# Kernel optimization log

Hardware: AMD Instinct MI355X
Metric: run time of the kernel (lower is better)

## Reference

```python
import jax, jax.numpy as jnp
import numpy as np

N, D_IN, D_OUT = 4096, 1024, 1024
DROPOUT_RATE = 0.1


def setup_inputs() -> dict:
    key = jax.random.key(0)
    kx, kq, kk, kv = jax.random.split(key, 4)
    s = 1.0 / np.sqrt(D_IN)
    return {
        "x": jax.random.normal(kx, (N, D_IN), dtype=jnp.float32),
        "wq": jax.random.normal(kq, (D_OUT, D_IN), dtype=jnp.float32) * s,
        "wk": jax.random.normal(kk, (D_OUT, D_IN), dtype=jnp.float32) * s,
        "wv": jax.random.normal(kv, (D_OUT, D_IN), dtype=jnp.float32) * s,
    }


def reference(x, wq, wk, wv):
    # torch Linear: y = x @ W.T  (no bias since qkv_bias=False)
    q = x @ wq.T                      # [N, d_out]
    k = x @ wk.T
    v = x @ wv.T
    scores = q @ k.T                  # [N, N]
    n = scores.shape[0]
    causal = jnp.tril(jnp.ones((n, n), dtype=bool))  # keep lower triangle
    masked = jnp.where(causal, scores, -jnp.inf)
    scale = k.shape[-1] ** 0.5
    weights = jax.nn.softmax(masked / scale, axis=-1)
    # dropout (train mode), fixed key for determinism
    keep = jax.random.bernoulli(jax.random.key(42), 1.0 - DROPOUT_RATE, weights.shape)
    weights = jnp.where(keep, weights / (1.0 - DROPOUT_RATE), 0.0)
    return weights @ v                # [N, d_out]
```

## Files before the change

### kernel.cpp

```cpp
#include <hip/hip_runtime.h>
#include <hip/hip_fp16.h>

typedef __attribute__((ext_vector_type(8))) _Float16 f16x8;
typedef __attribute__((ext_vector_type(4))) float f32x4;

typedef const __attribute__((address_space(1))) void gas_void;
typedef __attribute__((address_space(3))) void las_void;
typedef __attribute__((address_space(3))) const __half las_chalf;

__device__ __forceinline__ f16x8 ldsr(const __half* p) {
    f16x8 r;
    asm volatile("ds_read_b128 %0, %1" : "=v"(r) : "v"((las_chalf*)p));
    return r;
}

__global__ __launch_bounds__(256) void cast_f32_f16_k(const float* __restrict__ in,
                                                      __half* __restrict__ out, int n) {
    int i = (blockIdx.x * 256 + threadIdx.x) * 8;
    if (i >= n) return;
    float4 a = *(const float4*)(in + i);
    float4 b = *(const float4*)(in + i + 4);
    __half2 h[4] = { __floats2half2_rn(a.x, a.y), __floats2half2_rn(a.z, a.w),
                     __floats2half2_rn(b.x, b.y), __floats2half2_rn(b.z, b.w) };
    *(int4*)(out + i) = *(int4*)h;
}

__global__ __launch_bounds__(256) void cast3_f32_f16_k(const float* __restrict__ a,
                                                       const float* __restrict__ b,
                                                       const float* __restrict__ c,
                                                       __half* __restrict__ out) {
    const int which = blockIdx.x >> 9;
    const float* src = which == 0 ? a : (which == 1 ? b : c);
    const int i = (((blockIdx.x & 511) * 256) + threadIdx.x) * 8;
    float4 va = *(const float4*)(src + i);
    float4 vb = *(const float4*)(src + i + 4);
    __half2 h[4] = { __floats2half2_rn(va.x, va.y), __floats2half2_rn(va.z, va.w),
                     __floats2half2_rn(vb.x, vb.y), __floats2half2_rn(vb.z, vb.w) };
    *(int4*)(out + (size_t)which * 1048576 + i) = *(int4*)h;
}

__global__ __launch_bounds__(256) void transpose_f16_k(const __half* __restrict__ in,
                                                       __half* __restrict__ out,
                                                       int R, int ldin) {
    __shared__ __half t[64][72];
    int r0 = blockIdx.x * 64, c0 = blockIdx.y * 64;
    for (int idx = threadIdx.x; idx < 64 * 64; idx += 256) {
        int r = idx >> 6, c = idx & 63;
        t[r][c] = in[(size_t)(r0 + r) * ldin + c0 + c];
    }
    __syncthreads();
    for (int idx = threadIdx.x; idx < 64 * 64; idx += 256) {
        int r = idx >> 6, c = idx & 63;
        out[(size_t)(c0 + r) * R + r0 + c] = t[c][r];
    }
}

__device__ __forceinline__ void storeC(__half* C, size_t off, float v) { C[off] = __float2half(v); }
__device__ __forceinline__ void storeC(float*  C, size_t off, float v) { C[off] = v; }

template <typename CT, bool LOWER_ONLY, bool SPLITK>
__global__ __launch_bounds__(512, 2)
void gemm256(const __half* __restrict__ A, const __half* __restrict__ B, CT* __restrict__ C,
             float* __restrict__ P1, float* __restrict__ P2, float* __restrict__ P3,
             int lda, int ldb, int ldc, int NTin, float scale) {
    int bi, c = 0;
    const int bj = blockIdx.y;
    if (SPLITK) {
        int x = blockIdx.x;
        if (x < 4)       { bi = x;                    c = 0; }
        else if (x < 12) { bi = 4  + ((x - 4) >> 1);  c = (x - 4) & 1; }
        else if (x < 24) { bi = 8  + (x - 12) / 3;    c = (x - 12) % 3; }
        else             { bi = 12 + ((x - 24) >> 2); c = (x - 24) & 3; }
    } else {
        bi = blockIdx.x;
        if (LOWER_ONLY && bj > bi) return;
    }
    const int brow = bi * 256, bcol = bj * 256;
    const int tid = threadIdx.x;
    const int lane = tid & 63, wid = tid >> 6;
    const int wm = wid >> 2, wn = wid & 3;
    const int lane15 = lane & 15;
    const int kxor = (lane & 7) << 3;
    const int g16 = (lane >> 4) << 3;

    int k_lo = 0, NT = NTin;
    if (SPLITK) { int full = 4 * (bi + 1); k_lo = c * 16; NT = min(full - k_lo, 16); }

    extern __shared__ __half smem[];

    const int srow = (wid << 3) + (lane >> 3);
    const int scol = ((lane & 7) ^ ((lane >> 3) & 7)) << 3;

    auto stage_half = [&](const __half* G, int ldg, int growbase, int kt, int buf, int mat, int half) {
        const __half* src = G + (size_t)(growbase + half * 128 + srow) * ldg + kt * 64 + scol;
        __half* dst = &smem[buf * 32768 + mat * 16384 + (half * 128 + (wid << 3)) * 64];
        __builtin_amdgcn_global_load_lds((gas_void*)src, (las_void*)dst, 16, 0, 0);
        __builtin_amdgcn_global_load_lds((gas_void*)(src + (size_t)64 * ldg),
                                         (las_void*)(dst + 64 * 64), 16, 0, 0);
    };

    f32x4 acc[8][4] = {};
    f16x8 bfrag[2][4];

    stage_half(B, ldb, bcol, k_lo, 0, 1, 0);
    stage_half(B, ldb, bcol, k_lo, 0, 1, 1);
    stage_half(A, lda, brow, k_lo, 0, 0, 0);
    stage_half(A, lda, brow, k_lo, 0, 0, 1);
    if (NT > 1) {
        stage_half(B, ldb, bcol, k_lo + 1, 1, 1, 0);
        stage_half(B, ldb, bcol, k_lo + 1, 1, 1, 1);
    }

    for (int Tr = 0; Tr < NT; ++Tr) {
        const int Ta = k_lo + Tr;
        const int buf = Tr & 1;
        const __half* Abase = &smem[buf * 32768 + (wm * 128 + lane15) * 64];
        const __half* Bbase = &smem[buf * 32768 + 16384 + (wn * 64 + lane15) * 64];

        if (Tr < NT - 1) asm volatile("s_waitcnt vmcnt(4)" ::: "memory");
        else             asm volatile("s_waitcnt vmcnt(0)" ::: "memory");
        __builtin_amdgcn_s_barrier();

        {
#pragma unroll
            for (int kk = 0; kk < 2; ++kk)
#pragma unroll
                for (int n = 0; n < 4; ++n)
                    bfrag[kk][n] = ldsr(Bbase + (n * 16) * 64 + ((kk * 32 + g16) ^ kxor));
            f16x8 af[2][2];
#pragma unroll
            for (int mi = 0; mi < 2; ++mi)
#pragma unroll
                for (int kk = 0; kk < 2; ++kk)
                    af[mi][kk] = ldsr(Abase + (mi * 16) * 64 + ((kk * 32 + g16) ^ kxor));
            if (Tr + 1 < NT) stage_half(A, lda, brow, Ta + 1, buf ^ 1, 0, 0);
            asm volatile("s_waitcnt lgkmcnt(0)" ::: "memory");
            __builtin_amdgcn_sched_barrier(0);
            __builtin_amdgcn_s_setprio(1);
#pragma unroll
            for (int mi = 0; mi < 2; ++mi)
#pragma unroll
                for (int n = 0; n < 4; ++n)
#pragma unroll
                    for (int kk = 0; kk < 2; ++kk)
                        acc[mi][n] = __builtin_amdgcn_mfma_f32_16x16x32_f16(
                            af[mi][kk], bfrag[kk][n], acc[mi][n], 0, 0, 0);
            __builtin_amdgcn_s_setprio(0);
            __builtin_amdgcn_s_barrier();
        }

#pragma unroll
        for (int p = 1; p < 4; ++p) {
            f16x8 af[2][2];
#pragma unroll
            for (int mi = 0; mi < 2; ++mi)
#pragma unroll
                for (int kk = 0; kk < 2; ++kk)
                    af[mi][kk] = ldsr(Abase + ((2 * p + mi) * 16) * 64 + ((kk * 32 + g16) ^ kxor));
            if (p == 1)      { if (Tr + 1 < NT) stage_half(A, lda, brow, Ta + 1, buf ^ 1, 0, 1); }
            else if (p == 2) { if (Tr + 2 < NT) stage_half(B, ldb, bcol, Ta + 2, buf, 1, 0); }
            else             { if (Tr + 2 < NT) stage_half(B, ldb, bcol, Ta + 2, buf, 1, 1); }
            asm volatile("s_waitcnt lgkmcnt(0)" ::: "memory");
            __builtin_amdgcn_sched_barrier(0);
            __builtin_amdgcn_s_setprio(1);
#pragma unroll
            for (int mi = 0; mi < 2; ++mi)
#pragma unroll
                for (int n = 0; n < 4; ++n)
#pragma unroll
                    for (int kk = 0; kk < 2; ++kk)
                        acc[2 * p + mi][n] = __builtin_amdgcn_mfma_f32_16x16x32_f16(
                            af[mi][kk], bfrag[kk][n], acc[2 * p + mi][n], 0, 0, 0);
            __builtin_amdgcn_s_setprio(0);
            __builtin_amdgcn_s_barrier();
        }
    }

    CT* Ct = C;
    if (SPLITK && c > 0) Ct = (CT*)(c == 1 ? P1 : (c == 2 ? P2 : P3));
    const int r0 = (lane >> 4) << 2;
#pragma unroll
    for (int m = 0; m < 8; ++m) {
#pragma unroll
        for (int n = 0; n < 4; ++n) {
            int col = bcol + wn * 64 + n * 16 + lane15;
#pragma unroll
            for (int r = 0; r < 4; ++r) {
                int row = brow + wm * 128 + m * 16 + r0 + r;
                storeC(Ct, (size_t)row * ldc + col, acc[m][n][r] * scale);
            }
        }
    }
}

__global__ __launch_bounds__(256) void pv_reduce_k(float* __restrict__ out,
                                                   const float* __restrict__ P1,
                                                   const float* __restrict__ P2,
                                                   const float* __restrict__ P3) {
    const int row = 1024 + blockIdx.x;
    const size_t o = (size_t)row * 1024 + threadIdx.x * 4;
    float4 s = *(float4*)(out + o);
    float4 a = *(const float4*)(P1 + o);
    s.x += a.x; s.y += a.y; s.z += a.z; s.w += a.w;
    if (row >= 2048) {
        float4 b = *(const float4*)(P2 + o);
        s.x += b.x; s.y += b.y; s.z += b.z; s.w += b.w;
    }
    if (row >= 3072) {
        float4 d = *(const float4*)(P3 + o);
        s.x += d.x; s.y += d.y; s.z += d.z; s.w += d.w;
    }
    *(float4*)(out + o) = s;
}

__device__ __forceinline__ uint32_t rotl32(uint32_t x, int d) { return (x << d) | (x >> (32 - d)); }

__device__ __forceinline__ bool keep_bit(uint32_t i, uint32_t j) {
    uint32_t x0 = 0u;
    uint32_t x1 = i * 4096u + j;
    const uint32_t ks0 = 0u, ks1 = 42u, ks2 = 0u ^ 42u ^ 0x1BD11BDAu;
    x0 += ks0; x1 += ks1;
#define TFR(r) { x0 += x1; x1 = rotl32(x1, r); x1 ^= x0; }
    TFR(13) TFR(15) TFR(26) TFR(6)   x0 += ks1; x1 += ks2 + 1u;
    TFR(17) TFR(29) TFR(16) TFR(24)  x0 += ks2; x1 += ks0 + 2u;
    TFR(13) TFR(15) TFR(26) TFR(6)   x0 += ks0; x1 += ks1 + 3u;
    TFR(17) TFR(29) TFR(16) TFR(24)  x0 += ks1; x1 += ks2 + 4u;
    TFR(13) TFR(15) TFR(26) TFR(6)   x0 += ks2; x1 += ks0 + 5u;
#undef TFR
    uint32_t bits = x0 ^ x1;
    float u = __uint_as_float((bits >> 9) | 0x3f800000u) - 1.0f;
    return u < 0.9f;
}

__global__ __launch_bounds__(256) void softmax_dropout_k(__half* __restrict__ SP, int N) {
    const int i = blockIdx.x;
    const int tid = threadIdx.x;
    const int len = i + 1;
    __half* row = SP + (size_t)i * N;

    float m = -1.0e30f, l = 0.f;
    const int len8 = len & ~7;
    for (int j = tid * 8; j < len8; j += 2048) {
        int4 pk = *(const int4*)(row + j);
        const __half2* h2 = (const __half2*)&pk;
#pragma unroll
        for (int q = 0; q < 4; ++q) {
            float2 f2 = __half22float2(h2[q]);
            float nm = fmaxf(m, fmaxf(f2.x, f2.y));
            l = l * __expf(m - nm) + __expf(f2.x - nm) + __expf(f2.y - nm);
            m = nm;
        }
    }
    for (int j = len8 + tid; j < len; j += 256) {
        float s = __half2float(row[j]);
        float nm = fmaxf(m, s);
        l = l * __expf(m - nm) + __expf(s - nm);
        m = nm;
    }
    for (int off = 1; off < 64; off <<= 1) {
        float m2 = __shfl_xor(m, off);
        float l2 = __shfl_xor(l, off);
        float nm = fmaxf(m, m2);
        l = l * __expf(m - nm) + l2 * __expf(m2 - nm);
        m = nm;
    }
    __shared__ float ms[4], ls[4];
    if ((tid & 63) == 0) { ms[tid >> 6] = m; ls[tid >> 6] = l; }
    __syncthreads();
    float M = ms[0], L = ls[0];
#pragma unroll
    for (int w = 1; w < 4; ++w) {
        float nm = fmaxf(M, ms[w]);
        L = L * __expf(M - nm) + ls[w] * __expf(ms[w] - nm);
        M = nm;
    }
    const float inv = 1.0f / (L * 0.9f);

    for (int j = tid; j < len; j += 256) {
        float s = __half2float(row[j]);
        float w = __expf(s - M) * inv;
        row[j] = keep_bit((uint32_t)i, (uint32_t)j) ? __float2half(w) : __float2half(0.0f);
    }
    const int zlim = ((i >> 8) << 8) + 256;
    for (int j = len + tid; j < zlim; j += 256) row[j] = __float2half(0.0f);
}

extern "C" void kernel_launch(void* const* d_in, const int* in_sizes, int n_in,
                              void* d_out, int out_size, void* d_ws, size_t ws_size,
                              hipStream_t stream) {
    const float* x  = (const float*)d_in[0];
    const float* wq = (const float*)d_in[1];
    const float* wk = (const float*)d_in[2];
    const float* wv = (const float*)d_in[3];
    float* out = (float*)d_out;
    char* ws = (char*)d_ws;

    const int N = 4096, D = 1024;

    __half* xb   = (__half*)(ws + 0);
    __half* wqkv = (__half*)(ws + 8388608);
    __half* QKV  = (__half*)(ws + 14680064);
    __half* VT   = (__half*)(ws + 39845888);
    __half* SP   = (__half*)(ws + 48234496);

    float* P1 = (float*)(ws + 14680064) - (size_t)1024 * 1024;
    float* P2 = (float*)(ws + 14680064 + 12582912) - (size_t)2048 * 1024;
    float* P3 = (float*)(ws + 14680064 + 20971520) - (size_t)3072 * 1024;

    __half* Q = QKV;
    __half* K = QKV + 1024;
    __half* V = QKV + 2048;

    auto* gqkv_f = gemm256<__half, false, false>;
    auto* gs_f   = gemm256<__half, true,  false>;
    auto* gpv_f  = gemm256<float,  false, true>;
    (void)hipFuncSetAttribute((const void*)gqkv_f, hipFuncAttributeMaxDynamicSharedMemorySize, 131072);
    (void)hipFuncSetAttribute((const void*)gs_f,   hipFuncAttributeMaxDynamicSharedMemorySize, 131072);
    (void)hipFuncSetAttribute((const void*)gpv_f,  hipFuncAttributeMaxDynamicSharedMemorySize, 131072);

    cast_f32_f16_k<<<2048, 256, 0, stream>>>(x, xb, N * D);
    cast3_f32_f16_k<<<1536, 256, 0, stream>>>(wq, wk, wv, wqkv);

    dim3 gq(N / 256, 3 * D / 256);
    gqkv_f<<<gq, 512, 131072, stream>>>(xb, wqkv, QKV, nullptr, nullptr, nullptr,
                                        D, D, 3 * D, D / 64, 1.0f);

    dim3 gt(N / 64, D / 64);
    transpose_f16_k<<<gt, 256, 0, stream>>>(V, VT, N, 3 * D);

    dim3 gsd(N / 256, N / 256);
    gs_f<<<gsd, 512, 131072, stream>>>(Q, K, SP, nullptr, nullptr, nullptr,
                                       3 * D, 3 * D, N, D / 64, 0.03125f);

    softmax_dropout_k<<<N, 256, 0, stream>>>(SP, N);

    dim3 go(40, D / 256);
    gpv_f<<<go, 512, 131072, stream>>>(SP, VT, out, P1, P2, P3,
                                       N, N, D, 0, 1.0f);
    pv_reduce_k<<<3072, 256, 0, stream>>>(out, P1, P2, P3);
}
```

Measured before the change: 154.5 us.

## Compute softmax row max/sum in QK^T GEMM epilogue; vectorize softmax pass

The score GEMM now computes per-row, per-256-column-block max and exp-sum partials in its epilogue and writes them to a small workspace. The softmax kernel merges these partials instead of re-reading the row for a max/sum pass. Its normalize-and-dropout pass now uses 8-wide vectorized loads and stores, and it zeroes the tail with int4 stores. The two cast kernels are merged into one launch. Risks: extra epilogue work, shared-memory reuse, and register pressure in the score GEMM. Statistics are also computed from fp32 accumulators while the exp pass reads fp16-rounded scores, which adds a small numerical mismatch.

```diff
diff --git a/kernel.cpp b/kernel.cpp
--- a/kernel.cpp
+++ b/kernel.cpp
@@ -14,29 +14,30 @@
     return r;
 }
 
-__global__ __launch_bounds__(256) void cast_f32_f16_k(const float* __restrict__ in,
-                                                      __half* __restrict__ out, int n) {
-    int i = (blockIdx.x * 256 + threadIdx.x) * 8;
-    if (i >= n) return;
-    float4 a = *(const float4*)(in + i);
-    float4 b = *(const float4*)(in + i + 4);
+__global__ __launch_bounds__(256) void cast_all_k(const float* __restrict__ x,
+                                                  const float* __restrict__ wq,
+                                                  const float* __restrict__ wk,
+                                                  const float* __restrict__ wv,
+                                                  __half* __restrict__ xb,
+                                                  __half* __restrict__ wqkv) {
+    const int b = blockIdx.x;
+    const float* src;
+    __half* dst;
+    size_t i;
+    if (b < 2048) {
+        src = x; dst = xb;
+        i = ((size_t)b * 256 + threadIdx.x) * 8;
+    } else {
+        const int w = (b - 2048) >> 9;
+        src = w == 0 ? wq : (w == 1 ? wk : wv);
+        dst = wqkv + (size_t)w * 1048576;
+        i = (((size_t)((b - 2048) & 511)) * 256 + threadIdx.x) * 8;
+    }
+    float4 a = *(const float4*)(src + i);
+    float4 c = *(const float4*)(src + i + 4);
     __half2 h[4] = { __floats2half2_rn(a.x, a.y), __floats2half2_rn(a.z, a.w),
-                     __floats2half2_rn(b.x, b.y), __floats2half2_rn(b.z, b.w) };
-    *(int4*)(out + i) = *(int4*)h;
-}
-
-__global__ __launch_bounds__(256) void cast3_f32_f16_k(const float* __restrict__ a,
-                                                       const float* __restrict__ b,
-                                                       const float* __restrict__ c,
-                                                       __half* __restrict__ out) {
-    const int which = blockIdx.x >> 9;
-    const float* src = which == 0 ? a : (which == 1 ? b : c);
-    const int i = (((blockIdx.x & 511) * 256) + threadIdx.x) * 8;
-    float4 va = *(const float4*)(src + i);
-    float4 vb = *(const float4*)(src + i + 4);
-    __half2 h[4] = { __floats2half2_rn(va.x, va.y), __floats2half2_rn(va.z, va.w),
-                     __floats2half2_rn(vb.x, vb.y), __floats2half2_rn(vb.z, vb.w) };
-    *(int4*)(out + (size_t)which * 1048576 + i) = *(int4*)h;
+                     __floats2half2_rn(c.x, c.y), __floats2half2_rn(c.z, c.w) };
+    *(int4*)(dst + i) = *(int4*)h;
 }
 
 __global__ __launch_bounds__(256) void transpose_f16_k(const __half* __restrict__ in,
@@ -58,10 +59,11 @@
 __device__ __forceinline__ void storeC(__half* C, size_t off, float v) { C[off] = __float2half(v); }
 __device__ __forceinline__ void storeC(float*  C, size_t off, float v) { C[off] = v; }
 
-template <typename CT, bool LOWER_ONLY, bool SPLITK>
+template <typename CT, bool LOWER_ONLY, bool SPLITK, bool STATS>
 __global__ __launch_bounds__(512, 2)
 void gemm256(const __half* __restrict__ A, const __half* __restrict__ B, CT* __restrict__ C,
              float* __restrict__ P1, float* __restrict__ P2, float* __restrict__ P3,
+             float* __restrict__ Mp, float* __restrict__ Lp,
              int lda, int ldb, int ldc, int NTin, float scale) {
     int bi, c = 0;
     const int bj = blockIdx.y;
@@ -176,6 +178,56 @@
         }
     }
 
+    if (STATS) {
+        const bool diag = (bi == bj);
+        __syncthreads();
+        float* sst = (float*)smem;
+        const int g4 = lane >> 4;
+#pragma unroll
+        for (int m = 0; m < 8; ++m) {
+#pragma unroll
+            for (int r = 0; r < 4; ++r) {
+                const int lrow = wm * 128 + m * 16 + g4 * 4 + r;
+                const int grow = brow + lrow;
+                float v[4];
+                bool ok[4];
+                float mx = -1e30f;
+#pragma unroll
+                for (int n = 0; n < 4; ++n) {
+                    const int gcol = bcol + wn * 64 + n * 16 + lane15;
+                    v[n] = acc[m][n][r] * scale;
+                    ok[n] = (!diag) || (gcol <= grow);
+                    if (ok[n]) mx = fmaxf(mx, v[n]);
+                }
+#pragma unroll
+                for (int off = 1; off < 16; off <<= 1) mx = fmaxf(mx, __shfl_xor(mx, off));
+                float sm = 0.f;
+#pragma unroll
+                for (int n = 0; n < 4; ++n) if (ok[n]) sm += __expf(v[n] - mx);
+#pragma unroll
+                for (int off = 1; off < 16; off <<= 1) sm += __shfl_xor(sm, off);
+                if (lane15 == 0) {
+                    sst[(lrow * 4 + wn) * 2 + 0] = mx;
+                    sst[(lrow * 4 + wn) * 2 + 1] = sm;
+                }
+            }
+        }
+        __syncthreads();
+        if (tid < 256) {
+            float M2 = -1e30f, L2 = 0.f;
+#pragma unroll
+            for (int w = 0; w < 4; ++w) {
+                float m2 = sst[(tid * 4 + w) * 2 + 0];
+                float s2 = sst[(tid * 4 + w) * 2 + 1];
+                float nm2 = fmaxf(M2, m2);
+                L2 = L2 * __expf(M2 - nm2) + s2 * __expf(m2 - nm2);
+                M2 = nm2;
+            }
+            Mp[(size_t)(brow + tid) * 16 + bj] = M2;
+            Lp[(size_t)(brow + tid) * 16 + bj] = L2;
+        }
+    }
+
     CT* Ct = C;
     if (SPLITK && c > 0) Ct = (CT*)(c == 1 ? P1 : (c == 2 ? P2 : P3));
     const int r0 = (lane >> 4) << 2;
@@ -215,9 +267,9 @@
 
 __device__ __forceinline__ uint32_t rotl32(uint32_t x, int d) { return (x << d) | (x >> (32 - d)); }
 
-__device__ __forceinline__ bool keep_bit(uint32_t i, uint32_t j) {
+__device__ __forceinline__ bool keep_bit(uint32_t flat) {
     uint32_t x0 = 0u;
-    uint32_t x1 = i * 4096u + j;
+    uint32_t x1 = flat;
     const uint32_t ks0 = 0u, ks1 = 42u, ks2 = 0u ^ 42u ^ 0x1BD11BDAu;
     x0 += ks0; x1 += ks1;
 #define TFR(r) { x0 += x1; x1 = rotl32(x1, r); x1 ^= x0; }
@@ -232,57 +284,45 @@
     return u < 0.9f;
 }
 
-__global__ __launch_bounds__(256) void softmax_dropout_k(__half* __restrict__ SP, int N) {
+__global__ __launch_bounds__(256) void softmax_dropout_k(__half* __restrict__ SP,
+                                                         const float* __restrict__ Mp,
+                                                         const float* __restrict__ Lp,
+                                                         int N) {
     const int i = blockIdx.x;
     const int tid = threadIdx.x;
     const int len = i + 1;
     __half* row = SP + (size_t)i * N;
 
-    float m = -1.0e30f, l = 0.f;
+    const int nb = (i >> 8) + 1;
+    float M = -1e30f;
+    for (int b = 0; b < nb; ++b) M = fmaxf(M, Mp[(size_t)i * 16 + b]);
+    float L = 0.f;
+    for (int b = 0; b < nb; ++b) L += Lp[(size_t)i * 16 + b] * __expf(Mp[(size_t)i * 16 + b] - M);
+    const float inv = 1.0f / (L * 0.9f);
+
     const int len8 = len & ~7;
     for (int j = tid * 8; j < len8; j += 2048) {
         int4 pk = *(const int4*)(row + j);
-        const __half2* h2 = (const __half2*)&pk;
-#pragma unroll
-        for (int q = 0; q < 4; ++q) {
-            float2 f2 = __half22float2(h2[q]);
-            float nm = fmaxf(m, fmaxf(f2.x, f2.y));
-            l = l * __expf(m - nm) + __expf(f2.x - nm) + __expf(f2.y - nm);
-            m = nm;
-        }
+        const __half* hp = (const __half*)&pk;
+        __half o8[8];
+        const uint32_t base = (uint32_t)i * 4096u + (uint32_t)j;
+#pragma unroll
+        for (int q = 0; q < 8; ++q) {
+            float w = __expf(__half2float(hp[q]) - M) * inv;
+            o8[q] = keep_bit(base + q) ? __float2half(w) : __float2half(0.0f);
+        }
+        *(int4*)(row + j) = *(int4*)o8;
     }
     for (int j = len8 + tid; j < len; j += 256) {
-        float s = __half2float(row[j]);
-        float nm = fmaxf(m, s);
-        l = l * __expf(m - nm) + __expf(s - nm);
-        m = nm;
-    }
-    for (int off = 1; off < 64; off <<= 1) {
-        float m2 = __shfl_xor(m, off);
-        float l2 = __shfl_xor(l, off);
-        float nm = fmaxf(m, m2);
-        l = l * __expf(m - nm) + l2 * __expf(m2 - nm);
-        m = nm;
-    }
-    __shared__ float ms[4], ls[4];
-    if ((tid & 63) == 0) { ms[tid >> 6] = m; ls[tid >> 6] = l; }
-    __syncthreads();
-    float M = ms[0], L = ls[0];
-#pragma unroll
-    for (int w = 1; w < 4; ++w) {
-        float nm = fmaxf(M, ms[w]);
-        L = L * __expf(M - nm) + ls[w] * __expf(ms[w] - nm);
-        M = nm;
-    }
-    const float inv = 1.0f / (L * 0.9f);
-
-    for (int j = tid; j < len; j += 256) {
-        float s = __half2float(row[j]);
-        float w = __expf(s - M) * inv;
-        row[j] = keep_bit((uint32_t)i, (uint32_t)j) ? __float2half(w) : __float2half(0.0f);
-    }
+        float w = __expf(__half2float(row[j]) - M) * inv;
+        row[j] = keep_bit((uint32_t)i * 4096u + (uint32_t)j) ? __float2half(w) : __float2half(0.0f);
+    }
+
     const int zlim = ((i >> 8) << 8) + 256;
-    for (int j = len + tid; j < zlim; j += 256) row[j] = __float2half(0.0f);
+    const int za = (len + 7) & ~7;
+    for (int j = len + tid; j < min(za, zlim); j += 256) row[j] = __float2half(0.0f);
+    const int4 z = {0, 0, 0, 0};
+    for (int j = za + tid * 8; j < zlim; j += 2048) *(int4*)(row + j) = z;
 }
 
 extern "C" void kernel_launch(void* const* d_in, const int* in_sizes, int n_in,
@@ -302,6 +342,8 @@
     __half* QKV  = (__half*)(ws + 14680064);
     __half* VT   = (__half*)(ws + 39845888);
     __half* SP   = (__half*)(ws + 48234496);
+    float*  Mp   = (float*)(ws + 81788928);
+    float*  Lp   = (float*)(ws + 82051072);
 
     float* P1 = (float*)(ws + 14680064) - (size_t)1024 * 1024;
     float* P2 = (float*)(ws + 14680064 + 12582912) - (size_t)2048 * 1024;
@@ -311,31 +353,30 @@
     __half* K = QKV + 1024;
     __half* V = QKV + 2048;
 
-    auto* gqkv_f = gemm256<__half, false, false>;
-    auto* gs_f   = gemm256<__half, true,  false>;
-    auto* gpv_f  = gemm256<float,  false, true>;
+    auto* gqkv_f = gemm256<__half, false, false, false>;
+    auto* gs_f   = gemm256<__half, true,  false, true>;
+    auto* gpv_f  = gemm256<float,  false, true,  false>;
     (void)hipFuncSetAttribute((const void*)gqkv_f, hipFuncAttributeMaxDynamicSharedMemorySize, 131072);
     (void)hipFuncSetAttribute((const void*)gs_f,   hipFuncAttributeMaxDynamicSharedMemorySize, 131072);
     (void)hipFuncSetAttribute((const void*)gpv_f,  hipFuncAttributeMaxDynamicSharedMemorySize, 131072);
 
-    cast_f32_f16_k<<<2048, 256, 0, stream>>>(x, xb, N * D);
-    cast3_f32_f16_k<<<1536, 256, 0, stream>>>(wq, wk, wv, wqkv);
+    cast_all_k<<<3584, 256, 0, stream>>>(x, wq, wk, wv, xb, wqkv);
 
     dim3 gq(N / 256, 3 * D / 256);
     gqkv_f<<<gq, 512, 131072, stream>>>(xb, wqkv, QKV, nullptr, nullptr, nullptr,
-                                        D, D, 3 * D, D / 64, 1.0f);
+                                        nullptr, nullptr, D, D, 3 * D, D / 64, 1.0f);
 
     dim3 gt(N / 64, D / 64);
     transpose_f16_k<<<gt, 256, 0, stream>>>(V, VT, N, 3 * D);
 
     dim3 gsd(N / 256, N / 256);
     gs_f<<<gsd, 512, 131072, stream>>>(Q, K, SP, nullptr, nullptr, nullptr,
-                                       3 * D, 3 * D, N, D / 64, 0.03125f);
-
-    softmax_dropout_k<<<N, 256, 0, stream>>>(SP, N);
+                                       Mp, Lp, 3 * D, 3 * D, N, D / 64, 0.03125f);
+
+    softmax_dropout_k<<<N, 256, 0, stream>>>(SP, Mp, Lp, N);
 
     dim3 go(40, D / 256);
     gpv_f<<<go, 512, 131072, stream>>>(SP, VT, out, P1, P2, P3,
-                                       N, N, D, 0, 1.0f);
+                                       nullptr, nullptr, N, N, D, 0, 1.0f);
     pv_reduce_k<<<3072, 256, 0, stream>>>(out, P1, P2, P3);
 }
```

Measured after the change: 166.3 us. 7.7% more time.
